# Performance work log

Measured on AMD Instinct MI355X. Metric: run time of the kernel, lower is better.

Reference implementation:

```python
import jax, jax.numpy as jnp
import numpy as np

B, L, M, N = 1, 31, 1024, 1024


def setup_inputs() -> dict:
    key = jax.random.key(0)
    k1, k2 = jax.random.split(key)
    x = jax.random.normal(k1, (B, L, M, N), dtype=jnp.float32)   # spectral cube
    ca = jax.random.normal(k2, (1, 1, M, N), dtype=jnp.float32)  # coded aperture (mode='base')
    return {"x": x, "ca": ca}


def reference(x, ca):
    """CASSI base-mode forward: mask then prism shear + spectral sum.

    x:  (B, L, M, N) spectral scene
    ca: (1, 1, M, N) coded aperture
    returns (B, 1, M, N + L - 1) coded measurement
    """
    B_, L_, M_, N_ = x.shape
    y = x * ca  # (B, L, M, N) masked cube
    # band l contributes to output columns [l, l+N): vectorized shift-accumulate
    col = jnp.arange(L_)[:, None] + jnp.arange(N_)[None, :]  # (L, N) target columns
    out = jnp.zeros((B_, M_, N_ + L_ - 1), dtype=y.dtype)
    out = out.at[:, :, col].add(y.transpose(0, 2, 1, 3))  # values shape (B, M, L, N)
    return out[:, None, :, :]  # (B, 1, M, N + L - 1)
```

## Files before the change

kernel.cpp:

```cpp
#include <hip/hip_runtime.h>


constexpr int L = 31;
constexpr int M = 1024;
constexpr int N = 1024;
constexpr int NC = N + L - 1;
constexpr int LSTRIDE = M * N;
constexpr int BLK = 256;
constexpr int HALO = L - 1;
constexpr int CA_TILE = BLK + HALO;

__global__ __launch_bounds__(256) void cassi_fwd_kernel(
    const float* __restrict__ x,
    const float* __restrict__ ca,
    float* __restrict__ out)
{
    __shared__ float sca[CA_TILE];

    const int tid = threadIdx.x;
    const int C0  = blockIdx.x * BLK;
    const int m   = blockIdx.y;

    for (int i = tid; i < CA_TILE; i += BLK) {
        const int col = C0 - HALO + i;
        sca[i] = (col >= 0 && col < N) ? ca[m * N + col] : 0.0f;
    }
    __syncthreads();

    const int c = C0 + tid;
    if (c >= NC) return;

    const float* xp = x + m * N + c;

    float acc = 0.0f;
#pragma unroll
    for (int l = 0; l < L; ++l) {
        acc = fmaf(xp[l * LSTRIDE - l], sca[tid + HALO - l], acc);
    }

    out[m * NC + c] = acc;
}

extern "C" void kernel_launch(void* const* d_in, const int* in_sizes, int n_in,
                              void* d_out, int out_size, void* d_ws, size_t ws_size,
                              hipStream_t stream)
{
    const float* x  = (const float*)d_in[0];
    const float* ca = (const float*)d_in[1];
    float* out = (float*)d_out;

    dim3 block(BLK, 1, 1);
    dim3 grid((NC + BLK - 1) / BLK, M, 1);
    cassi_fwd_kernel<<<grid, block, 0, stream>>>(x, ca, out);
}
```

Before: 28.77 us.

## Process four rows per thread with interleaved float4 shared aperture tile

Each block now handles four image rows instead of one. The coded-aperture tile is stored in shared memory as interleaved float4, so a single LDS read serves all four rows. Each thread keeps four accumulators, which gives it more independent loads in flight and cuts the block count by four. The grid shrinks, which lowers occupancy and parallelism, and register pressure rises.

```diff
diff --git a/kernel.cpp b/kernel.cpp
--- a/kernel.cpp
+++ b/kernel.cpp
@@ -7,38 +7,51 @@
 constexpr int NC = N + L - 1;
 constexpr int LSTRIDE = M * N;
 constexpr int BLK = 256;
+constexpr int ROWS = 4;
 constexpr int HALO = L - 1;
 constexpr int CA_TILE = BLK + HALO;
 
-__global__ __launch_bounds__(256) void cassi_fwd_kernel(
+typedef float f32x4 __attribute__((ext_vector_type(4)));
+
+__global__ __launch_bounds__(BLK) void cassi_fwd_kernel(
     const float* __restrict__ x,
     const float* __restrict__ ca,
     float* __restrict__ out)
 {
-    __shared__ float sca[CA_TILE];
+    __shared__ f32x4 scaT[CA_TILE];
 
     const int tid = threadIdx.x;
     const int C0  = blockIdx.x * BLK;
-    const int m   = blockIdx.y;
+    const int m0  = blockIdx.y * ROWS;
 
-    for (int i = tid; i < CA_TILE; i += BLK) {
-        const int col = C0 - HALO + i;
-        sca[i] = (col >= 0 && col < N) ? ca[m * N + col] : 0.0f;
+    for (int idx = tid; idx < CA_TILE * ROWS; idx += BLK) {
+        const int w   = idx >> 2;
+        const int i   = idx & 3;
+        const int col = C0 - HALO + w;
+        float v = 0.0f;
+        if (col >= 0 && col < N) v = ca[(m0 + i) * N + col];
+        ((float*)scaT)[idx] = v;
     }
     __syncthreads();
 
     const int c = C0 + tid;
     if (c >= NC) return;
 
-    const float* xp = x + m * N + c;
+    const float* xp = x + m0 * N + c;
 
-    float acc = 0.0f;
+    float acc[ROWS] = {0.f, 0.f, 0.f, 0.f};
 #pragma unroll
     for (int l = 0; l < L; ++l) {
-        acc = fmaf(xp[l * LSTRIDE - l], sca[tid + HALO - l], acc);
+        const f32x4 cav = scaT[tid + HALO - l];
+        const long  o   = (long)l * LSTRIDE - l;
+#pragma unroll
+        for (int i = 0; i < ROWS; ++i)
+            acc[i] = fmaf(xp[o + i * N], cav[i], acc[i]);
     }
 
-    out[m * NC + c] = acc;
+    float* op = out + (long)m0 * NC + c;
+#pragma unroll
+    for (int i = 0; i < ROWS; ++i) op[i * NC] = acc[i];
 }
 
 extern "C" void kernel_launch(void* const* d_in, const int* in_sizes, int n_in,
@@ -50,6 +63,6 @@
     float* out = (float*)d_out;
 
     dim3 block(BLK, 1, 1);
-    dim3 grid((NC + BLK - 1) / BLK, M, 1);
+    dim3 grid((NC + BLK - 1) / BLK, M / ROWS, 1);
     cassi_fwd_kernel<<<grid, block, 0, stream>>>(x, ca, out);
 }
```

Result: slower. 29.38 us (+2.1%).

## Switch to input-stationary float4 scatter with shared-memory column reduction

Applied to the files above, without the earlier changes.

Each block now handles one full row, and each thread loads float4 chunks of x and ca with aligned vector loads instead of unaligned scalar reads at shifted offsets. Each thread accumulates into 34 private partial sums, writes them to a padded shared-memory buffer, and the block gathers the overlapping partials per output column. This targets the misaligned shifted loads and the redundant ca halo handling, at the cost of a ~35 KB shared buffer, lower occupancy and a serial per-column reduction loop.

```diff
diff --git a/kernel.cpp b/kernel.cpp
--- a/kernel.cpp
+++ b/kernel.cpp
@@ -7,38 +7,52 @@
 constexpr int NC = N + L - 1;
 constexpr int LSTRIDE = M * N;
 constexpr int BLK = 256;
-constexpr int HALO = L - 1;
-constexpr int CA_TILE = BLK + HALO;
+constexpr int ACCW = 4 + (L - 1);
+constexpr int PAD = 35;
 
-__global__ __launch_bounds__(256) void cassi_fwd_kernel(
+typedef float f32x4 __attribute__((ext_vector_type(4)));
+
+__global__ __launch_bounds__(BLK, 4) void cassi_fwd_kernel(
     const float* __restrict__ x,
     const float* __restrict__ ca,
     float* __restrict__ out)
 {
-    __shared__ float sca[CA_TILE];
+    __shared__ float red[BLK * PAD];
 
-    const int tid = threadIdx.x;
-    const int C0  = blockIdx.x * BLK;
-    const int m   = blockIdx.y;
+    const int t = threadIdx.x;
+    const int m = blockIdx.x;
 
-    for (int i = tid; i < CA_TILE; i += BLK) {
-        const int col = C0 - HALO + i;
-        sca[i] = (col >= 0 && col < N) ? ca[m * N + col] : 0.0f;
+    f32x4 cav;
+    __builtin_memcpy(&cav, ca + m * N + 4 * t, 16);
+
+    float acc[ACCW];
+#pragma unroll
+    for (int k = 0; k < ACCW; ++k) acc[k] = 0.0f;
+
+    const float* xp = x + m * N + 4 * t;
+#pragma unroll
+    for (int l = 0; l < L; ++l) {
+        f32x4 q;
+        __builtin_memcpy(&q, xp + (long)l * LSTRIDE, 16);
+#pragma unroll
+        for (int j = 0; j < 4; ++j)
+            acc[l + j] = fmaf(q[j], cav[j], acc[l + j]);
     }
+
+#pragma unroll
+    for (int k = 0; k < ACCW; ++k) red[t * PAD + k] = acc[k];
     __syncthreads();
 
-    const int c = C0 + tid;
-    if (c >= NC) return;
-
-    const float* xp = x + m * N + c;
-
-    float acc = 0.0f;
-#pragma unroll
-    for (int l = 0; l < L; ++l) {
-        acc = fmaf(xp[l * LSTRIDE - l], sca[tid + HALO - l], acc);
+    for (int c = t; c < NC; c += BLK) {
+        int tlo = (c - 30) >> 2;
+        if (tlo < 0) tlo = 0;
+        int thi = c >> 2;
+        if (thi > BLK - 1) thi = BLK - 1;
+        float s = 0.0f;
+        for (int tt = tlo; tt <= thi; ++tt)
+            s += red[tt * PAD + (c - 4 * tt)];
+        out[(long)m * NC + c] = s;
     }
-
-    out[m * NC + c] = acc;
 }
 
 extern "C" void kernel_launch(void* const* d_in, const int* in_sizes, int n_in,
@@ -50,6 +64,6 @@
     float* out = (float*)d_out;
 
     dim3 block(BLK, 1, 1);
-    dim3 grid((NC + BLK - 1) / BLK, M, 1);
+    dim3 grid(M, 1, 1);
     cassi_fwd_kernel<<<grid, block, 0, stream>>>(x, ca, out);
 }
```

Result: slower. 30.72 us (+6.8%).

## Split tail columns into mini blocks and give each main thread two columns

Applied to the files above, without the earlier changes.

The 30 tail columns past N are handled by 128 small blocks that each cover 8 rows. The remaining columns use 2048 blocks of 512 columns, with each thread computing two outputs 256 apart. This removes the mostly idle fifth column-block per row that the old grid launched. Block indices are swizzled across rows, and launch bounds request 8 blocks per SM. The cost is divergent mini blocks that read x and ca directly without shared-memory staging.

```diff
diff --git a/kernel.cpp b/kernel.cpp
--- a/kernel.cpp
+++ b/kernel.cpp
@@ -8,37 +8,60 @@
 constexpr int LSTRIDE = M * N;
 constexpr int BLK = 256;
 constexpr int HALO = L - 1;
-constexpr int CA_TILE = BLK + HALO;
+constexpr int W = 512;
+constexpr int CA_TILE = W + HALO;
+constexpr int NMINI = 128;
+constexpr int NMAIN = 2 * M;
 
-__global__ __launch_bounds__(256) void cassi_fwd_kernel(
+__global__ __launch_bounds__(BLK, 8) void cassi_fwd_kernel(
     const float* __restrict__ x,
     const float* __restrict__ ca,
     float* __restrict__ out)
 {
+    const int i = blockIdx.x;
+    const int t = threadIdx.x;
+
+    if (i < NMINI) {
+        if (t < 240) {
+            const int r = t / 30;
+            const int c = N + (t - 30 * r);
+            const int m = 8 * i + r;
+            const int llo = c - (N - 1);
+            float a = 0.0f;
+            for (int l = llo; l < L; ++l) {
+                const int col = c - l;
+                a = fmaf(x[(long)l * LSTRIDE + m * N + col],
+                         ca[m * N + col], a);
+            }
+            out[m * NC + c] = a;
+        }
+        return;
+    }
+
+    const int j  = i - NMINI;
+    const int jj = (j & 7) * (NMAIN / 8) + (j >> 3);
+    const int m  = jj >> 1;
+    const int C0 = (jj & 1) * W;
+
     __shared__ float sca[CA_TILE];
-
-    const int tid = threadIdx.x;
-    const int C0  = blockIdx.x * BLK;
-    const int m   = blockIdx.y;
-
-    for (int i = tid; i < CA_TILE; i += BLK) {
-        const int col = C0 - HALO + i;
-        sca[i] = (col >= 0 && col < N) ? ca[m * N + col] : 0.0f;
+    for (int k = t; k < CA_TILE; k += BLK) {
+        const int col = C0 - HALO + k;
+        sca[k] = ((unsigned)col < (unsigned)N) ? ca[m * N + col] : 0.0f;
     }
     __syncthreads();
 
-    const int c = C0 + tid;
-    if (c >= NC) return;
-
-    const float* xp = x + m * N + c;
-
-    float acc = 0.0f;
+    const float* xp = x + m * N + C0 + t;
+    float a0 = 0.0f, a1 = 0.0f;
 #pragma unroll
     for (int l = 0; l < L; ++l) {
-        acc = fmaf(xp[l * LSTRIDE - l], sca[tid + HALO - l], acc);
+        const long o = (long)l * LSTRIDE - l;
+        a0 = fmaf(xp[o],       sca[t + HALO - l],       a0);
+        a1 = fmaf(xp[o + 256], sca[t + 256 + HALO - l], a1);
     }
 
-    out[m * NC + c] = acc;
+    float* op = out + m * NC + C0 + t;
+    op[0]   = a0;
+    op[256] = a1;
 }
 
 extern "C" void kernel_launch(void* const* d_in, const int* in_sizes, int n_in,
@@ -50,6 +73,6 @@
     float* out = (float*)d_out;
 
     dim3 block(BLK, 1, 1);
-    dim3 grid((NC + BLK - 1) / BLK, M, 1);
+    dim3 grid(NMINI + NMAIN, 1, 1);
     cassi_fwd_kernel<<<grid, block, 0, stream>>>(x, ca, out);
 }
```

New measurement: 27.81 us. -3.4%, faster.
